# Performance work log

Hardware: AMD Instinct MI355X
Metric: run time of the kernel (lower is better)

The kernel has to match this reference:

```python
import jax, jax.numpy as jnp
import numpy as np

NUM_BINS = 15
N, C = 524288, 100


def setup_inputs() -> dict:
    key = jax.random.key(0)
    k1, k2 = jax.random.split(key)
    logits = jax.random.normal(k1, (N, C), dtype=jnp.float32)
    labels = jax.random.randint(k2, (N,), 0, C, dtype=jnp.int64)
    return {"logits": logits, "labels": labels}


def reference(logits, labels):
    # softmax over classes
    outputs = jax.nn.softmax(logits, axis=1)                      # [N, C]
    # per-sample prob of the true class and the max (confidence)
    pred_probs = jnp.take_along_axis(outputs, labels[:, None].astype(jnp.int32), axis=1)[:, 0]  # [N]
    max_probs = jnp.max(outputs, axis=1)                          # [N]
    # bin assignment: floor(p / (1/num_bins)) clamped to [0, num_bins-1]
    bin_idx = jnp.clip(jnp.floor(max_probs * NUM_BINS).astype(jnp.int32), 0, NUM_BINS - 1)
    # single-pass histogram via segment_sum (replaces per-bin masked loop)
    ones = jnp.ones_like(max_probs)
    counts = jax.ops.segment_sum(ones, bin_idx, num_segments=NUM_BINS)       # [B]
    sum_conf = jax.ops.segment_sum(max_probs, bin_idx, num_segments=NUM_BINS)
    sum_acc = jax.ops.segment_sum(pred_probs, bin_idx, num_segments=NUM_BINS)
    nonempty = counts > 0
    safe_counts = jnp.where(nonempty, counts, 1.0)
    bin_conf = jnp.where(nonempty, sum_conf / safe_counts, 0.0)
    bin_acc = jnp.where(nonempty, sum_acc / safe_counts, 0.0)
    ece = jnp.sum(counts * jnp.abs(bin_conf - bin_acc)) / jnp.sum(counts)
    return ece
```

## Files before the change

kernel.cpp:

```cpp
#include <hip/hip_runtime.h>
#include <math.h>

#define NUM_BINS 15
#define CCLS 100
#define GRID 2048
#define BLOCK 256

__global__ __launch_bounds__(BLOCK) void ece_fused(
    const float* __restrict__ logits,
    const int* __restrict__ labels,
    float* __restrict__ ws,
    float* __restrict__ out,
    int n_rows)
{
    __shared__ float s_cnt[NUM_BINS], s_conf[NUM_BINS], s_acc[NUM_BINS];
    __shared__ int s_last;

    const int tid = threadIdx.x;
    if (tid < NUM_BINS) { s_cnt[tid] = 0.f; s_conf[tid] = 0.f; s_acc[tid] = 0.f; }
    __syncthreads();

    const int lane = tid & 63;
    const int g    = lane >> 4;
    const int s    = lane & 15;
    const int wave = tid >> 6;
    const int gwave = blockIdx.x * (BLOCK / 64) + wave;
    const int nwav  = GRID * (BLOCK / 64);
    const int n_chunks = n_rows >> 3;
    const bool hasb = (s < 9);

    for (int chunk = gwave; chunk < n_chunks; chunk += nwav) {
        const int r0 = (chunk << 3) + g;
        const int r1 = r0 + 4;
        const float* p0 = logits + (size_t)r0 * CCLS;
        const float* p1 = logits + (size_t)r1 * CCLS;

        float4 a0 = *(const float4*)(p0 + 4 * s);
        float4 a1 = *(const float4*)(p1 + 4 * s);
        float4 b0 = a0, b1 = a1;
        if (hasb) {
            b0 = *(const float4*)(p0 + 64 + 4 * s);
            b1 = *(const float4*)(p1 + 64 + 4 * s);
        }
        int lab0 = 0, lab1 = 0;
        if (s == 0) { lab0 = labels[r0]; lab1 = labels[r1]; }

        float m0 = fmaxf(fmaxf(a0.x, a0.y), fmaxf(a0.z, a0.w));
        float m1 = fmaxf(fmaxf(a1.x, a1.y), fmaxf(a1.z, a1.w));
        float e0 = __expf(a0.x) + __expf(a0.y) + __expf(a0.z) + __expf(a0.w);
        float e1 = __expf(a1.x) + __expf(a1.y) + __expf(a1.z) + __expf(a1.w);
        if (hasb) {
            m0 = fmaxf(m0, fmaxf(fmaxf(b0.x, b0.y), fmaxf(b0.z, b0.w)));
            m1 = fmaxf(m1, fmaxf(fmaxf(b1.x, b1.y), fmaxf(b1.z, b1.w)));
            e0 += __expf(b0.x) + __expf(b0.y) + __expf(b0.z) + __expf(b0.w);
            e1 += __expf(b1.x) + __expf(b1.y) + __expf(b1.z) + __expf(b1.w);
        }

        #pragma unroll
        for (int off = 8; off >= 1; off >>= 1) {
            m0 = fmaxf(m0, __shfl_xor(m0, off));
            m1 = fmaxf(m1, __shfl_xor(m1, off));
            e0 += __shfl_xor(e0, off);
            e1 += __shfl_xor(e1, off);
        }

        if (s == 0) {
            const float xl0 = p0[lab0];
            const float xl1 = p1[lab1];
            const float inv0 = 1.0f / e0, inv1 = 1.0f / e1;
            const float conf0 = __expf(m0) * inv0;
            const float conf1 = __expf(m1) * inv1;
            const float pred0 = __expf(xl0) * inv0;
            const float pred1 = __expf(xl1) * inv1;
            int bin0 = (int)(conf0 * (float)NUM_BINS); bin0 = bin0 > NUM_BINS - 1 ? NUM_BINS - 1 : bin0;
            int bin1 = (int)(conf1 * (float)NUM_BINS); bin1 = bin1 > NUM_BINS - 1 ? NUM_BINS - 1 : bin1;
            atomicAdd(&s_cnt[bin0], 1.f); atomicAdd(&s_conf[bin0], conf0); atomicAdd(&s_acc[bin0], pred0);
            atomicAdd(&s_cnt[bin1], 1.f); atomicAdd(&s_conf[bin1], conf1); atomicAdd(&s_acc[bin1], pred1);
        }
    }

    if (gwave == 0) {
        for (int r = (n_chunks << 3) + g; r < n_rows; r += 4) {
            const float* p = logits + (size_t)r * CCLS;
            float4 a = *(const float4*)(p + 4 * s);
            float m = fmaxf(fmaxf(a.x, a.y), fmaxf(a.z, a.w));
            float e = __expf(a.x) + __expf(a.y) + __expf(a.z) + __expf(a.w);
            if (hasb) {
                float4 b = *(const float4*)(p + 64 + 4 * s);
                m = fmaxf(m, fmaxf(fmaxf(b.x, b.y), fmaxf(b.z, b.w)));
                e += __expf(b.x) + __expf(b.y) + __expf(b.z) + __expf(b.w);
            }
            #pragma unroll
            for (int off = 8; off >= 1; off >>= 1) {
                m = fmaxf(m, __shfl_xor(m, off));
                e += __shfl_xor(e, off);
            }
            if (s == 0) {
                const float inv = 1.0f / e;
                const float conf = __expf(m) * inv;
                const float pred = __expf(p[labels[r]]) * inv;
                int bin = (int)(conf * (float)NUM_BINS); bin = bin > NUM_BINS - 1 ? NUM_BINS - 1 : bin;
                atomicAdd(&s_cnt[bin], 1.f); atomicAdd(&s_conf[bin], conf); atomicAdd(&s_acc[bin], pred);
            }
        }
    }

    __syncthreads();
    if (tid < NUM_BINS) {
        atomicAdd(&ws[tid],                s_cnt[tid]);
        atomicAdd(&ws[NUM_BINS + tid],     s_conf[tid]);
        atomicAdd(&ws[2 * NUM_BINS + tid], s_acc[tid]);
    }
    __syncthreads();

    if (tid == 0) {
        __threadfence();
        const int t = atomicAdd((int*)(ws + 48), 1);
        s_last = (t == GRID - 1) ? 1 : 0;
    }
    __syncthreads();
    if (s_last && tid < 64) {
        __threadfence();
        float contrib = 0.f, cnt = 0.f;
        if (tid < NUM_BINS) {
            cnt = __hip_atomic_load(&ws[tid],                __ATOMIC_RELAXED, __HIP_MEMORY_SCOPE_AGENT);
            const float sc = __hip_atomic_load(&ws[NUM_BINS + tid],     __ATOMIC_RELAXED, __HIP_MEMORY_SCOPE_AGENT);
            const float sa = __hip_atomic_load(&ws[2 * NUM_BINS + tid], __ATOMIC_RELAXED, __HIP_MEMORY_SCOPE_AGENT);
            if (cnt > 0.f) contrib = cnt * fabsf(sc / cnt - sa / cnt);
        }
        #pragma unroll
        for (int off = 32; off >= 1; off >>= 1) {
            contrib += __shfl_xor(contrib, off);
            cnt     += __shfl_xor(cnt, off);
        }
        if (tid == 0) out[0] = contrib / cnt;
    }
}

extern "C" void kernel_launch(void* const* d_in, const int* in_sizes, int n_in,
                              void* d_out, int out_size, void* d_ws, size_t ws_size,
                              hipStream_t stream)
{
    const float* logits = (const float*)d_in[0];
    const int*   labels = (const int*)d_in[1];
    float* out = (float*)d_out;
    float* ws  = (float*)d_ws;

    const int n_rows = in_sizes[1];

    hipMemsetAsync(ws, 0, 64 * sizeof(float), stream);

    ece_fused<<<dim3(GRID), dim3(BLOCK), 0, stream>>>(logits, labels, ws, out, n_rows);
}
```

Before: 370.7 us.

## Accumulate per-bin confidence-accuracy differences in registers instead of shared atomics

```diff
diff --git a/kernel.cpp b/kernel.cpp
--- a/kernel.cpp
+++ b/kernel.cpp
@@ -6,6 +6,12 @@
 #define GRID 2048
 #define BLOCK 256
 
+__device__ __forceinline__ float pick4(float4 v, int i) {
+    float lo = (i & 1) ? v.y : v.x;
+    float hi = (i & 1) ? v.w : v.z;
+    return (i & 2) ? hi : lo;
+}
+
 __global__ __launch_bounds__(BLOCK) void ece_fused(
     const float* __restrict__ logits,
     const int* __restrict__ labels,
@@ -13,13 +19,10 @@
     float* __restrict__ out,
     int n_rows)
 {
-    __shared__ float s_cnt[NUM_BINS], s_conf[NUM_BINS], s_acc[NUM_BINS];
+    __shared__ float s_part[(BLOCK / 64) * 16];
     __shared__ int s_last;
 
-    const int tid = threadIdx.x;
-    if (tid < NUM_BINS) { s_cnt[tid] = 0.f; s_conf[tid] = 0.f; s_acc[tid] = 0.f; }
-    __syncthreads();
-
+    const int tid  = threadIdx.x;
     const int lane = tid & 63;
     const int g    = lane >> 4;
     const int s    = lane & 15;
@@ -28,6 +31,8 @@
     const int nwav  = GRID * (BLOCK / 64);
     const int n_chunks = n_rows >> 3;
     const bool hasb = (s < 9);
+
+    float dacc = 0.f;
 
     for (int chunk = gwave; chunk < n_chunks; chunk += nwav) {
         const int r0 = (chunk << 3) + g;
@@ -42,8 +47,8 @@
             b0 = *(const float4*)(p0 + 64 + 4 * s);
             b1 = *(const float4*)(p1 + 64 + 4 * s);
         }
-        int lab0 = 0, lab1 = 0;
-        if (s == 0) { lab0 = labels[r0]; lab1 = labels[r1]; }
+        const int lab0 = labels[r0];
+        const int lab1 = labels[r1];
 
         float m0 = fmaxf(fmaxf(a0.x, a0.y), fmaxf(a0.z, a0.w));
         float m1 = fmaxf(fmaxf(a1.x, a1.y), fmaxf(a1.z, a1.w));
@@ -56,61 +61,72 @@
             e1 += __expf(b1.x) + __expf(b1.y) + __expf(b1.z) + __expf(b1.w);
         }
 
+        const int la0 = lab0 >> 2, lo0 = lab0 & 3;
+        const int la1 = lab1 >> 2, lo1 = lab1 & 3;
+        float t0 = 0.f, t1 = 0.f;
+        if (la0 == s)           t0 = __expf(pick4(a0, lo0));
+        else if (la0 - 16 == s) t0 = __expf(pick4(b0, lo0));
+        if (la1 == s)           t1 = __expf(pick4(a1, lo1));
+        else if (la1 - 16 == s) t1 = __expf(pick4(b1, lo1));
+
         #pragma unroll
         for (int off = 8; off >= 1; off >>= 1) {
             m0 = fmaxf(m0, __shfl_xor(m0, off));
             m1 = fmaxf(m1, __shfl_xor(m1, off));
             e0 += __shfl_xor(e0, off);
             e1 += __shfl_xor(e1, off);
+            t0 += __shfl_xor(t0, off);
+            t1 += __shfl_xor(t1, off);
         }
 
-        if (s == 0) {
-            const float xl0 = p0[lab0];
-            const float xl1 = p1[lab1];
-            const float inv0 = 1.0f / e0, inv1 = 1.0f / e1;
-            const float conf0 = __expf(m0) * inv0;
-            const float conf1 = __expf(m1) * inv1;
-            const float pred0 = __expf(xl0) * inv0;
-            const float pred1 = __expf(xl1) * inv1;
-            int bin0 = (int)(conf0 * (float)NUM_BINS); bin0 = bin0 > NUM_BINS - 1 ? NUM_BINS - 1 : bin0;
-            int bin1 = (int)(conf1 * (float)NUM_BINS); bin1 = bin1 > NUM_BINS - 1 ? NUM_BINS - 1 : bin1;
-            atomicAdd(&s_cnt[bin0], 1.f); atomicAdd(&s_conf[bin0], conf0); atomicAdd(&s_acc[bin0], pred0);
-            atomicAdd(&s_cnt[bin1], 1.f); atomicAdd(&s_conf[bin1], conf1); atomicAdd(&s_acc[bin1], pred1);
-        }
+        const float inv0 = 1.0f / e0, inv1 = 1.0f / e1;
+        const float conf0 = __expf(m0) * inv0, conf1 = __expf(m1) * inv1;
+        const float diff0 = conf0 - t0 * inv0;
+        const float diff1 = conf1 - t1 * inv1;
+        int bin0 = (int)(conf0 * (float)NUM_BINS); bin0 = bin0 > NUM_BINS - 1 ? NUM_BINS - 1 : bin0;
+        int bin1 = (int)(conf1 * (float)NUM_BINS); bin1 = bin1 > NUM_BINS - 1 ? NUM_BINS - 1 : bin1;
+        dacc += (s == bin0) ? diff0 : 0.f;
+        dacc += (s == bin1) ? diff1 : 0.f;
     }
 
     if (gwave == 0) {
         for (int r = (n_chunks << 3) + g; r < n_rows; r += 4) {
             const float* p = logits + (size_t)r * CCLS;
             float4 a = *(const float4*)(p + 4 * s);
+            float4 b = a;
+            if (hasb) b = *(const float4*)(p + 64 + 4 * s);
+            const int lab = labels[r];
             float m = fmaxf(fmaxf(a.x, a.y), fmaxf(a.z, a.w));
             float e = __expf(a.x) + __expf(a.y) + __expf(a.z) + __expf(a.w);
             if (hasb) {
-                float4 b = *(const float4*)(p + 64 + 4 * s);
                 m = fmaxf(m, fmaxf(fmaxf(b.x, b.y), fmaxf(b.z, b.w)));
                 e += __expf(b.x) + __expf(b.y) + __expf(b.z) + __expf(b.w);
             }
+            const int la = lab >> 2, lo = lab & 3;
+            float t = 0.f;
+            if (la == s)           t = __expf(pick4(a, lo));
+            else if (la - 16 == s) t = __expf(pick4(b, lo));
             #pragma unroll
             for (int off = 8; off >= 1; off >>= 1) {
                 m = fmaxf(m, __shfl_xor(m, off));
                 e += __shfl_xor(e, off);
+                t += __shfl_xor(t, off);
             }
-            if (s == 0) {
-                const float inv = 1.0f / e;
-                const float conf = __expf(m) * inv;
-                const float pred = __expf(p[labels[r]]) * inv;
-                int bin = (int)(conf * (float)NUM_BINS); bin = bin > NUM_BINS - 1 ? NUM_BINS - 1 : bin;
-                atomicAdd(&s_cnt[bin], 1.f); atomicAdd(&s_conf[bin], conf); atomicAdd(&s_acc[bin], pred);
-            }
+            const float inv = 1.0f / e;
+            const float conf = __expf(m) * inv;
+            const float diff = conf - t * inv;
+            int bin = (int)(conf * (float)NUM_BINS); bin = bin > NUM_BINS - 1 ? NUM_BINS - 1 : bin;
+            dacc += (s == bin) ? diff : 0.f;
         }
     }
 
+    dacc += __shfl_xor(dacc, 16);
+    dacc += __shfl_xor(dacc, 32);
+    if (lane < 16) s_part[wave * 16 + lane] = dacc;
     __syncthreads();
-    if (tid < NUM_BINS) {
-        atomicAdd(&ws[tid],                s_cnt[tid]);
-        atomicAdd(&ws[NUM_BINS + tid],     s_conf[tid]);
-        atomicAdd(&ws[2 * NUM_BINS + tid], s_acc[tid]);
-    }
+
+    if (tid < NUM_BINS)
+        atomicAdd(&ws[tid], s_part[tid] + s_part[16 + tid] + s_part[32 + tid] + s_part[48 + tid]);
     __syncthreads();
 
     if (tid == 0) {
@@ -121,19 +137,15 @@
     __syncthreads();
     if (s_last && tid < 64) {
         __threadfence();
-        float contrib = 0.f, cnt = 0.f;
+        float contrib = 0.f;
         if (tid < NUM_BINS) {
-            cnt = __hip_atomic_load(&ws[tid],                __ATOMIC_RELAXED, __HIP_MEMORY_SCOPE_AGENT);
-            const float sc = __hip_atomic_load(&ws[NUM_BINS + tid],     __ATOMIC_RELAXED, __HIP_MEMORY_SCOPE_AGENT);
-            const float sa = __hip_atomic_load(&ws[2 * NUM_BINS + tid], __ATOMIC_RELAXED, __HIP_MEMORY_SCOPE_AGENT);
-            if (cnt > 0.f) contrib = cnt * fabsf(sc / cnt - sa / cnt);
+            const float v = __hip_atomic_load(&ws[tid], __ATOMIC_RELAXED, __HIP_MEMORY_SCOPE_AGENT);
+            contrib = fabsf(v);
         }
         #pragma unroll
-        for (int off = 32; off >= 1; off >>= 1) {
+        for (int off = 32; off >= 1; off >>= 1)
             contrib += __shfl_xor(contrib, off);
-            cnt     += __shfl_xor(cnt, off);
-        }
-        if (tid == 0) out[0] = contrib / cnt;
+        if (tid == 0) out[0] = contrib / (float)n_rows;
     }
 }
 
```

Result: no change. 377.1 us (+1.7%).
